# Optimization experiments

Hardware: AMD Instinct MI355X
Metric: run time of the kernel (lower is better)

The kernel has to match this reference:

```python
import jax, jax.numpy as jnp
import numpy as np

H = 50  # LSTM units
T = 10  # NUMBARS
F = 5   # input features
B = 131072


def _lstm(x, W, U, b):
    """Keras-default LSTM. x: [B,T,Fin], W: [Fin,4H], U: [H,4H], b: [4H].
    Gate order i,f,g(c),o; sigmoid recurrent act, tanh cell act, zero init state.
    Returns (all_h [B,T,H], last_h [B,H])."""
    Bn = x.shape[0]
    h0 = jnp.zeros((Bn, H), x.dtype)
    c0 = jnp.zeros((Bn, H), x.dtype)

    def step(carry, xt):
        h, c = carry
        z = xt @ W + h @ U + b  # [B,4H]
        i, f, g, o = jnp.split(z, 4, axis=-1)
        i = jax.nn.sigmoid(i)
        f = jax.nn.sigmoid(f)
        g = jnp.tanh(g)
        o = jax.nn.sigmoid(o)
        c_new = f * c + i * g
        h_new = o * jnp.tanh(c_new)
        return (h_new, c_new), h_new

    (h_last, _), hs = jax.lax.scan(step, (h0, c0), jnp.swapaxes(x, 0, 1))
    return jnp.swapaxes(hs, 0, 1), h_last


def setup_inputs() -> dict:
    key = jax.random.key(0)
    ks = jax.random.split(key, 16)
    d = {"x": jax.random.normal(ks[0], (B, T, F), dtype=jnp.float32)}
    in_dims = [F, H, H, H]
    for l in range(4):
        s_in = 1.0 / np.sqrt(in_dims[l])
        s_h = 1.0 / np.sqrt(H)
        d[f"W{l+1}"] = jax.random.normal(ks[1 + 3 * l], (in_dims[l], 4 * H), dtype=jnp.float32) * s_in
        d[f"U{l+1}"] = jax.random.normal(ks[2 + 3 * l], (H, 4 * H), dtype=jnp.float32) * s_h
        # Keras unit_forget_bias: forget-gate bias = 1
        b = jnp.zeros((4 * H,), jnp.float32).at[H:2 * H].set(1.0)
        d[f"b{l+1}"] = b
    d["Wd1"] = jax.random.normal(ks[13], (H, 50), dtype=jnp.float32) * (1.0 / np.sqrt(H))
    d["bd1"] = jnp.zeros((50,), jnp.float32)
    d["Wd2"] = jax.random.normal(ks[14], (50, 1), dtype=jnp.float32) * (1.0 / np.sqrt(50))
    d["bd2"] = jnp.zeros((1,), jnp.float32)
    return d


def reference(x, W1, U1, b1, W2, U2, b2, W3, U3, b3, W4, U4, b4, Wd1, bd1, Wd2, bd2):
    # Dropout layers are identity at inference (Keras default training=False).
    h, _ = _lstm(x, W1, U1, b1)
    h, _ = _lstm(h, W2, U2, b2)
    h, _ = _lstm(h, W3, U3, b3)
    _, h = _lstm(h, W4, U4, b4)        # return_sequences=False -> last h [B,H]
    h = h @ Wd1 + bd1                   # Dense(50), linear activation
    out = jax.nn.sigmoid(h @ Wd2 + bd2) # Dense(1, sigmoid) -> [B,1]
    return out
```

## Files before the change

### kernel.cpp

```cpp
#include <hip/hip_runtime.h>


typedef __attribute__((ext_vector_type(8))) short short8;
typedef __attribute__((ext_vector_type(4))) float floatx4;
typedef __attribute__((ext_vector_type(2))) float float2v;
typedef unsigned short u16;
typedef unsigned int u32;

constexpr int H_ = 50, T_ = 10, F_ = 5;
constexpr int MTILE = 64;
constexpr int BLKT = 256;
constexpr float LOG2E = 1.4426950408889634f;

__device__ __forceinline__ float rcp_(float x) { return __builtin_amdgcn_rcpf(x); }
__device__ __forceinline__ float exp2_(float x) { return __builtin_amdgcn_exp2f(x); }
__device__ __forceinline__ float sig_nat(float x) {
  return rcp_(1.0f + exp2_(-LOG2E * x));
}

__device__ __forceinline__ u16 f2bf(float f) {
  union { float f; unsigned u; } v; v.f = f;
  unsigned r = v.u + 0x7FFFu + ((v.u >> 16) & 1u);
  return (u16)(r >> 16);
}
__device__ __forceinline__ float bf2f(u16 s) {
  union { unsigned u; float f; } v; v.u = ((unsigned)s) << 16;
  return v.f;
}
__device__ __forceinline__ unsigned pk_bf16(float a, float b) {
  return (unsigned)f2bf(a) | ((unsigned)f2bf(b) << 16);
}

__global__ void prep_kernel(
    const float* W1, const float* U1, const float* b1, const float* W2,
    const float* U2, const float* b2, const float* W3, const float* U3,
    const float* b3, const float* W4, const float* U4, const float* b4,
    const float* Wd1, const float* bd1, const float* Wd2, const float* bd2,
    u16* Wpp, float* biasP, float* vdense) {
  int idx = blockIdx.x * blockDim.x + threadIdx.x;
  const float* Wt[4] = {W1, W2, W3, W4};
  const float* Ut[4] = {U1, U2, U3, U4};
  const float* bt[4] = {b1, b2, b3, b4};
  const int fin[4] = {F_, H_, H_, H_};
  if (idx < 4 * 32768) {
    int l = idx >> 15, r = idx & 32767;
    int j = r & 7, lane = (r >> 3) & 63, w = (r >> 9) & 3, gI = (r >> 11) & 3,
        kt = r >> 13;
    int row = kt * 32 + (lane >> 4) * 8 + j;
    int u = w * 16 + (lane & 15);
    float val = 0.0f;
    if (u < H_) {
      if (row < 64) {
        if (row < fin[l]) val = Wt[l][row * 200 + gI * H_ + u];
      } else {
        int rr = row - 64;
        if (rr < H_) val = Ut[l][rr * 200 + gI * H_ + u];
      }
    }
    val *= (gI == 2) ? (2.0f * LOG2E) : (-LOG2E);
    Wpp[idx] = f2bf(val);
  } else if (idx < 4 * 32768 + 1024) {
    int r = idx - 4 * 32768;
    int l = r >> 8, q = r & 255, gI = q >> 6, u = q & 63;
    float val = (u < H_) ? bt[l][gI * H_ + u] : 0.0f;
    biasP[r] = val * ((gI == 2) ? (2.0f * LOG2E) : (-LOG2E));
  } else if (idx < 4 * 32768 + 1024 + 51) {
    int u = idx - (4 * 32768 + 1024);
    if (u < H_) {
      float s = 0.0f;
      for (int n = 0; n < H_; ++n) s += Wd1[u * H_ + n] * Wd2[n];
      vdense[u] = s;
    } else {
      float s = bd2[0];
      for (int n = 0; n < H_; ++n) s += bd1[n] * Wd2[n];
      vdense[50] = s;
    }
  }
}

template <bool FIRST, bool LAST>
__global__ __launch_bounds__(BLKT, 2) void lstm_mfma(
    const float* __restrict__ x0, u16* hbuf, const u16* __restrict__ Wpp,
    const float* __restrict__ biasP, int nblk, const float* __restrict__ vdense,
    float* __restrict__ out) {
  __shared__ __align__(16) u16 A[8192];
  const int tid = threadIdx.x;
  const int w = tid >> 6, lane = tid & 63;
  const int np = lane & 15, quad = lane >> 4;
  const int blk = blockIdx.x;
  const int b0 = blk * MTILE;
  const int u = w * 16 + np;

  short8 bfr[4][4];
#pragma unroll
  for (int kt = 0; kt < 4; ++kt)
#pragma unroll
    for (int gI = 0; gI < 4; ++gI)
      bfr[kt][gI] = *(const short8*)&Wpp[(((kt * 4 + gI) * 4 + w) * 64 + lane) * 8];

  float bv[4];
#pragma unroll
  for (int gI = 0; gI < 4; ++gI) bv[gI] = biasP[gI * 64 + u];

  for (int i = tid; i < 4096; i += BLKT) ((u32*)A)[i] = 0;

  float2v cst[8];
#pragma unroll
  for (int i = 0; i < 8; ++i) cst[i] = float2v{0.0f, 0.0f};

  short8 rx0, rx1;
  if constexpr (!FIRST) {
    const u16* s0 = hbuf + ((size_t)0 * nblk + blk) * 4096;
    rx0 = *(const short8*)(s0 + (size_t)tid * 8);
    rx1 = *(const short8*)(s0 + (size_t)(tid + 256) * 8);
  }

  const int kt_u = 2 + (w >> 1);
  const int cbase = ((kt_u * 4 + ((w & 1) * 2 + (np >> 3))) * 16 + quad * 4) * 8 + (np & 7);

  __syncthreads();

#pragma unroll 1
  for (int t = 0; t < T_; ++t) {
    if constexpr (!FIRST) {
      {
        int hc = tid, mt = hc >> 7, kk = (hc >> 6) & 1, rest = hc & 63;
        *(short8*)&A[((mt * 4 + kk) * 64 + rest) * 8] = rx0;
      }
      {
        int hc = tid + 256, mt = hc >> 7, kk = (hc >> 6) & 1, rest = hc & 63;
        *(short8*)&A[((mt * 4 + kk) * 64 + rest) * 8] = rx1;
      }
      if (t + 1 < T_) {
        const u16* s1 = hbuf + ((size_t)(t + 1) * nblk + blk) * 4096;
        rx0 = *(const short8*)(s1 + (size_t)tid * 8);
        rx1 = *(const short8*)(s1 + (size_t)(tid + 256) * 8);
      }
    } else {
      for (int e = tid; e < MTILE * F_; e += BLKT) {
        int row = e / F_, k = e - row * F_;
        int mt = row >> 4, rr = row & 15;
        A[(mt * 256 + rr) * 8 + k] =
            f2bf(x0[(size_t)(b0 + row) * (T_ * F_) + t * F_ + k]);
      }
    }
    __syncthreads();

    floatx4 acc[4][4];
#pragma unroll
    for (int mt = 0; mt < 4; ++mt)
#pragma unroll
      for (int gI = 0; gI < 4; ++gI)
        acc[mt][gI] = floatx4{bv[gI], bv[gI], bv[gI], bv[gI]};

#pragma unroll
    for (int kt = 0; kt < 4; ++kt) {
      if (FIRST && kt == 1) continue;
#pragma unroll
      for (int mt = 0; mt < 4; ++mt) {
        short8 af = *(const short8*)&A[(((mt * 4 + kt) * 4 + quad) * 16 + np) * 8];
#pragma unroll
        for (int gI = 0; gI < 4; ++gI)
          acc[mt][gI] = __builtin_amdgcn_mfma_f32_16x16x32_bf16(
              af, bfr[kt][gI], acc[mt][gI], 0, 0, 0);
      }
    }
    __syncthreads();

#pragma unroll
    for (int mt = 0; mt < 4; ++mt) {
#pragma unroll
      for (int p = 0; p < 2; ++p) {
        float2v di = {exp2_(acc[mt][0][2 * p]), exp2_(acc[mt][0][2 * p + 1])};
        float2v df = {exp2_(acc[mt][1][2 * p]), exp2_(acc[mt][1][2 * p + 1])};
        float2v dg = {exp2_(acc[mt][2][2 * p]), exp2_(acc[mt][2][2 * p + 1])};
        float2v do_ = {exp2_(acc[mt][3][2 * p]), exp2_(acc[mt][3][2 * p + 1])};
        di += 1.0f; df += 1.0f; dg += 1.0f; do_ += 1.0f;
        float2v m1 = di * df, m2 = do_ * dg;
        float2v P = m1 * m2;
        float Rs = rcp_(P.x * P.y);
        float2v R = {Rs * P.y, Rs * P.x};
        float2v i_ = (df * m2) * R;
        float2v f_ = (di * m2) * R;
        float2v o_ = (m1 * dg) * R;
        float2v g_ = 1.0f - 2.0f * ((m1 * do_) * R);
        float2v cn = f_ * cst[mt * 2 + p] + i_ * g_;
        cst[mt * 2 + p] = cn;
        float2v s = cn * (2.0f * LOG2E);
        float2v dc = {exp2_(s.x), exp2_(s.y)};
        dc += 1.0f;
        float Rc = rcp_(dc.x * dc.y);
        float2v tc = 1.0f - 2.0f * float2v{Rc * dc.y, Rc * dc.x};
        float2v h = o_ * tc;
        unsigned pk = pk_bf16(h.x, h.y);
        int a0 = cbase + mt * 2048 + (2 * p) * 8;
        A[a0] = (u16)pk;
        A[a0 + 8] = (u16)(pk >> 16);
      }
    }

    if constexpr (!LAST) {
      u16* dst = hbuf + ((size_t)t * nblk + blk) * 4096;
#pragma unroll
      for (int rep = 0; rep < 2; ++rep) {
        int e = lane + 64 * rep;
        int mt = e >> 5, rem = e & 31, qp = rem >> 4, rr = rem & 15;
        int quad_u = (w & 1) * 2 + qp;
        int ldsc = ((mt * 4 + kt_u) * 4 + quad_u) * 16 + rr;
        int hch = ((mt * 2 + (w >> 1)) * 4 + quad_u) * 16 + rr;
        *(short8*)&dst[(size_t)hch * 8] = *(const short8*)&A[ldsc * 8];
      }
    }
  }

  if constexpr (LAST) {
    __syncthreads();
    if (tid < MTILE) {
      int mt = tid >> 4, rr = tid & 15;
      float s = vdense[50];
      for (int k = 0; k < H_; ++k) {
        int ktu = 2 + (k >> 5), qd = (k & 31) >> 3, j = k & 7;
        s += bf2f(A[(((mt * 4 + ktu) * 4 + qd) * 16 + rr) * 8 + j]) * vdense[k];
      }
      out[b0 + tid] = sig_nat(s);
    }
  }
}

extern "C" void kernel_launch(void* const* d_in, const int* in_sizes, int n_in,
                              void* d_out, int out_size, void* d_ws,
                              size_t ws_size, hipStream_t stream) {
  const float* x = (const float*)d_in[0];
  const float* W1 = (const float*)d_in[1];
  const float* U1 = (const float*)d_in[2];
  const float* b1 = (const float*)d_in[3];
  const float* W2 = (const float*)d_in[4];
  const float* U2 = (const float*)d_in[5];
  const float* b2 = (const float*)d_in[6];
  const float* W3 = (const float*)d_in[7];
  const float* U3 = (const float*)d_in[8];
  const float* b3 = (const float*)d_in[9];
  const float* W4 = (const float*)d_in[10];
  const float* U4 = (const float*)d_in[11];
  const float* b4 = (const float*)d_in[12];
  const float* Wd1 = (const float*)d_in[13];
  const float* bd1 = (const float*)d_in[14];
  const float* Wd2 = (const float*)d_in[15];
  const float* bd2 = (const float*)d_in[16];

  const int Bn = in_sizes[0] / (T_ * F_);
  const int nblk = Bn / MTILE;
  char* ws = (char*)d_ws;
  u16* hbuf = (u16*)ws;
  size_t off = (size_t)T_ * nblk * 4096 * sizeof(u16);
  u16* Wpp = (u16*)(ws + off);
  float* biasP = (float*)(ws + off + 262144);
  float* vdense = (float*)(ws + off + 262144 + 4096);
  float* out = (float*)d_out;

  prep_kernel<<<(4 * 32768 + 1024 + 51 + 255) / 256, 256, 0, stream>>>(
      W1, U1, b1, W2, U2, b2, W3, U3, b3, W4, U4, b4, Wd1, bd1, Wd2, bd2, Wpp,
      biasP, vdense);

  dim3 grid(nblk), blkd(BLKT);
  lstm_mfma<true, false><<<grid, blkd, 0, stream>>>(
      x, hbuf, Wpp + 0 * 32768, biasP + 0 * 256, nblk, vdense, nullptr);
  lstm_mfma<false, false><<<grid, blkd, 0, stream>>>(
      nullptr, hbuf, Wpp + 1 * 32768, biasP + 1 * 256, nblk, vdense, nullptr);
  lstm_mfma<false, false><<<grid, blkd, 0, stream>>>(
      nullptr, hbuf, Wpp + 2 * 32768, biasP + 2 * 256, nblk, vdense, nullptr);
  lstm_mfma<false, true><<<grid, blkd, 0, stream>>>(
      nullptr, hbuf, Wpp + 3 * 32768, biasP + 3 * 256, nblk, vdense, out);
}
```

Baseline: 572.2 us.

## Fuse all four LSTM layers into one kernel keeping hidden sequences in LDS

Replaces four per-layer kernel launches that pass hidden sequences through a global bf16 buffer with a single kernel. Each block keeps all ten timesteps of hidden state in shared memory and runs the layers back to back, overwriting each timestep slot in place. The tile shrinks from 64 to 32 rows with a launch bound of three blocks per CU. This removes global round-trips and launch overhead, at the cost of more shared memory per block, fewer rows per MFMA batch, and per-layer weight reloads.

```diff
diff --git a/kernel.cpp b/kernel.cpp
--- a/kernel.cpp
+++ b/kernel.cpp
@@ -8,7 +8,7 @@
 typedef unsigned int u32;
 
 constexpr int H_ = 50, T_ = 10, F_ = 5;
-constexpr int MTILE = 64;
+constexpr int MTILE = 32;
 constexpr int BLKT = 256;
 constexpr float LOG2E = 1.4426950408889634f;
 
@@ -78,152 +78,147 @@
   }
 }
 
-template <bool FIRST, bool LAST>
-__global__ __launch_bounds__(BLKT, 2) void lstm_mfma(
-    const float* __restrict__ x0, u16* hbuf, const u16* __restrict__ Wpp,
-    const float* __restrict__ biasP, int nblk, const float* __restrict__ vdense,
+__global__ __launch_bounds__(BLKT, 3) void lstm_fused(
+    const float* __restrict__ x0, const u16* __restrict__ Wpp,
+    const float* __restrict__ biasP, const float* __restrict__ vdense,
     float* __restrict__ out) {
-  __shared__ __align__(16) u16 A[8192];
+  __shared__ __align__(16) u16 buf[T_ * 2048];
+  __shared__ __align__(16) u16 xb[T_ * 256];
+  __shared__ __align__(16) u16 zc[8];
+
   const int tid = threadIdx.x;
   const int w = tid >> 6, lane = tid & 63;
   const int np = lane & 15, quad = lane >> 4;
-  const int blk = blockIdx.x;
-  const int b0 = blk * MTILE;
+  const int b0 = blockIdx.x * MTILE;
   const int u = w * 16 + np;
 
-  short8 bfr[4][4];
-#pragma unroll
-  for (int kt = 0; kt < 4; ++kt)
-#pragma unroll
-    for (int gI = 0; gI < 4; ++gI)
-      bfr[kt][gI] = *(const short8*)&Wpp[(((kt * 4 + gI) * 4 + w) * 64 + lane) * 8];
-
-  float bv[4];
-#pragma unroll
-  for (int gI = 0; gI < 4; ++gI) bv[gI] = biasP[gI * 64 + u];
-
-  for (int i = tid; i < 4096; i += BLKT) ((u32*)A)[i] = 0;
-
-  float2v cst[8];
-#pragma unroll
-  for (int i = 0; i < 8; ++i) cst[i] = float2v{0.0f, 0.0f};
-
-  short8 rx0, rx1;
-  if constexpr (!FIRST) {
-    const u16* s0 = hbuf + ((size_t)0 * nblk + blk) * 4096;
-    rx0 = *(const short8*)(s0 + (size_t)tid * 8);
-    rx1 = *(const short8*)(s0 + (size_t)(tid + 256) * 8);
-  }
-
-  const int kt_u = 2 + (w >> 1);
-  const int cbase = ((kt_u * 4 + ((w & 1) * 2 + (np >> 3))) * 16 + quad * 4) * 8 + (np & 7);
-
+  for (int i = tid; i < T_ * 128; i += BLKT) ((u32*)xb)[i] = 0;
+  if (tid < 4) ((u32*)zc)[tid] = 0;
   __syncthreads();
 
+  for (int e = tid; e < MTILE * 50; e += BLKT) {
+    int row = e / 50, q = e - row * 50;
+    int t = q / 5, f = q - t * 5;
+    xb[t * 256 + row * 8 + f] = f2bf(x0[(size_t)(b0 + row) * 50 + q]);
+  }
+  __syncthreads();
+
+  const int rbase = quad * 128 + np * 8;
+  const int cb0 = (w >> 1) * 512 + ((w & 1) * 2 + (np >> 3)) * 128 + quad * 32 + (np & 7);
+
+  float2v cst[4];
+
 #pragma unroll 1
-  for (int t = 0; t < T_; ++t) {
-    if constexpr (!FIRST) {
-      {
-        int hc = tid, mt = hc >> 7, kk = (hc >> 6) & 1, rest = hc & 63;
-        *(short8*)&A[((mt * 4 + kk) * 64 + rest) * 8] = rx0;
-      }
-      {
-        int hc = tid + 256, mt = hc >> 7, kk = (hc >> 6) & 1, rest = hc & 63;
-        *(short8*)&A[((mt * 4 + kk) * 64 + rest) * 8] = rx1;
-      }
-      if (t + 1 < T_) {
-        const u16* s1 = hbuf + ((size_t)(t + 1) * nblk + blk) * 4096;
-        rx0 = *(const short8*)(s1 + (size_t)tid * 8);
-        rx1 = *(const short8*)(s1 + (size_t)(tid + 256) * 8);
-      }
-    } else {
-      for (int e = tid; e < MTILE * F_; e += BLKT) {
-        int row = e / F_, k = e - row * F_;
-        int mt = row >> 4, rr = row & 15;
-        A[(mt * 256 + rr) * 8 + k] =
-            f2bf(x0[(size_t)(b0 + row) * (T_ * F_) + t * F_ + k]);
-      }
-    }
-    __syncthreads();
-
-    floatx4 acc[4][4];
-#pragma unroll
-    for (int mt = 0; mt < 4; ++mt)
-#pragma unroll
-      for (int gI = 0; gI < 4; ++gI)
-        acc[mt][gI] = floatx4{bv[gI], bv[gI], bv[gI], bv[gI]};
-
-#pragma unroll
-    for (int kt = 0; kt < 4; ++kt) {
-      if (FIRST && kt == 1) continue;
-#pragma unroll
-      for (int mt = 0; mt < 4; ++mt) {
-        short8 af = *(const short8*)&A[(((mt * 4 + kt) * 4 + quad) * 16 + np) * 8];
-#pragma unroll
-        for (int gI = 0; gI < 4; ++gI)
-          acc[mt][gI] = __builtin_amdgcn_mfma_f32_16x16x32_bf16(
-              af, bfr[kt][gI], acc[mt][gI], 0, 0, 0);
-      }
-    }
-    __syncthreads();
-
-#pragma unroll
-    for (int mt = 0; mt < 4; ++mt) {
-#pragma unroll
-      for (int p = 0; p < 2; ++p) {
-        float2v di = {exp2_(acc[mt][0][2 * p]), exp2_(acc[mt][0][2 * p + 1])};
-        float2v df = {exp2_(acc[mt][1][2 * p]), exp2_(acc[mt][1][2 * p + 1])};
-        float2v dg = {exp2_(acc[mt][2][2 * p]), exp2_(acc[mt][2][2 * p + 1])};
-        float2v do_ = {exp2_(acc[mt][3][2 * p]), exp2_(acc[mt][3][2 * p + 1])};
-        di += 1.0f; df += 1.0f; dg += 1.0f; do_ += 1.0f;
-        float2v m1 = di * df, m2 = do_ * dg;
-        float2v P = m1 * m2;
-        float Rs = rcp_(P.x * P.y);
-        float2v R = {Rs * P.y, Rs * P.x};
-        float2v i_ = (df * m2) * R;
-        float2v f_ = (di * m2) * R;
-        float2v o_ = (m1 * dg) * R;
-        float2v g_ = 1.0f - 2.0f * ((m1 * do_) * R);
-        float2v cn = f_ * cst[mt * 2 + p] + i_ * g_;
-        cst[mt * 2 + p] = cn;
-        float2v s = cn * (2.0f * LOG2E);
-        float2v dc = {exp2_(s.x), exp2_(s.y)};
-        dc += 1.0f;
-        float Rc = rcp_(dc.x * dc.y);
-        float2v tc = 1.0f - 2.0f * float2v{Rc * dc.y, Rc * dc.x};
-        float2v h = o_ * tc;
-        unsigned pk = pk_bf16(h.x, h.y);
-        int a0 = cbase + mt * 2048 + (2 * p) * 8;
-        A[a0] = (u16)pk;
-        A[a0 + 8] = (u16)(pk >> 16);
-      }
-    }
-
-    if constexpr (!LAST) {
-      u16* dst = hbuf + ((size_t)t * nblk + blk) * 4096;
-#pragma unroll
-      for (int rep = 0; rep < 2; ++rep) {
-        int e = lane + 64 * rep;
-        int mt = e >> 5, rem = e & 31, qp = rem >> 4, rr = rem & 15;
-        int quad_u = (w & 1) * 2 + qp;
-        int ldsc = ((mt * 4 + kt_u) * 4 + quad_u) * 16 + rr;
-        int hch = ((mt * 2 + (w >> 1)) * 4 + quad_u) * 16 + rr;
-        *(short8*)&dst[(size_t)hch * 8] = *(const short8*)&A[ldsc * 8];
-      }
-    }
-  }
-
-  if constexpr (LAST) {
-    __syncthreads();
-    if (tid < MTILE) {
-      int mt = tid >> 4, rr = tid & 15;
-      float s = vdense[50];
-      for (int k = 0; k < H_; ++k) {
-        int ktu = 2 + (k >> 5), qd = (k & 31) >> 3, j = k & 7;
-        s += bf2f(A[(((mt * 4 + ktu) * 4 + qd) * 16 + rr) * 8 + j]) * vdense[k];
-      }
-      out[b0 + tid] = sig_nat(s);
-    }
+  for (int l = 0; l < 4; ++l) {
+    const u16* wp = Wpp + l * 32768;
+    short8 bfr[4][4];
+#pragma unroll
+    for (int kt = 0; kt < 4; ++kt)
+#pragma unroll
+      for (int g = 0; g < 4; ++g)
+        bfr[kt][g] = *(const short8*)&wp[(((kt * 4 + g) * 4 + w) * 64 + lane) * 8];
+    float bv[4];
+#pragma unroll
+    for (int g = 0; g < 4; ++g) bv[g] = biasP[l * 256 + g * 64 + u];
+#pragma unroll
+    for (int i = 0; i < 4; ++i) cst[i] = float2v{0.0f, 0.0f};
+
+#pragma unroll 1
+    for (int t = 0; t < T_; ++t) {
+      u16* bt = &buf[t * 2048];
+      const u16* bp = &buf[(t == 0 ? 0 : (t - 1)) * 2048];
+
+      floatx4 acc[2][4];
+#pragma unroll
+      for (int mt = 0; mt < 2; ++mt)
+#pragma unroll
+        for (int g = 0; g < 4; ++g)
+          acc[mt][g] = floatx4{bv[g], bv[g], bv[g], bv[g]};
+
+      if (l == 0) {
+#pragma unroll
+        for (int mt = 0; mt < 2; ++mt) {
+          const u16* ap = (quad == 0) ? &xb[t * 256 + (mt * 16 + np) * 8] : zc;
+          short8 af = *(const short8*)ap;
+#pragma unroll
+          for (int g = 0; g < 4; ++g)
+            acc[mt][g] = __builtin_amdgcn_mfma_f32_16x16x32_bf16(
+                af, bfr[0][g], acc[mt][g], 0, 0, 0);
+        }
+      } else {
+#pragma unroll
+        for (int mt = 0; mt < 2; ++mt) {
+          short8 a0 = *(const short8*)&bt[mt * 1024 + rbase];
+          short8 a1 = *(const short8*)&bt[mt * 1024 + 512 + rbase];
+#pragma unroll
+          for (int g = 0; g < 4; ++g) {
+            acc[mt][g] = __builtin_amdgcn_mfma_f32_16x16x32_bf16(
+                a0, bfr[0][g], acc[mt][g], 0, 0, 0);
+            acc[mt][g] = __builtin_amdgcn_mfma_f32_16x16x32_bf16(
+                a1, bfr[1][g], acc[mt][g], 0, 0, 0);
+          }
+        }
+      }
+      if (t > 0) {
+#pragma unroll
+        for (int mt = 0; mt < 2; ++mt) {
+          short8 h0 = *(const short8*)&bp[mt * 1024 + rbase];
+          short8 h1 = *(const short8*)&bp[mt * 1024 + 512 + rbase];
+#pragma unroll
+          for (int g = 0; g < 4; ++g) {
+            acc[mt][g] = __builtin_amdgcn_mfma_f32_16x16x32_bf16(
+                h0, bfr[2][g], acc[mt][g], 0, 0, 0);
+            acc[mt][g] = __builtin_amdgcn_mfma_f32_16x16x32_bf16(
+                h1, bfr[3][g], acc[mt][g], 0, 0, 0);
+          }
+        }
+      }
+      if (l > 0) __syncthreads();
+
+#pragma unroll
+      for (int mt = 0; mt < 2; ++mt) {
+#pragma unroll
+        for (int p = 0; p < 2; ++p) {
+          float2v di = {exp2_(acc[mt][0][2 * p]), exp2_(acc[mt][0][2 * p + 1])};
+          float2v df = {exp2_(acc[mt][1][2 * p]), exp2_(acc[mt][1][2 * p + 1])};
+          float2v dg = {exp2_(acc[mt][2][2 * p]), exp2_(acc[mt][2][2 * p + 1])};
+          float2v do_ = {exp2_(acc[mt][3][2 * p]), exp2_(acc[mt][3][2 * p + 1])};
+          di += 1.0f; df += 1.0f; dg += 1.0f; do_ += 1.0f;
+          float2v m1 = di * df, m2 = do_ * dg;
+          float2v P = m1 * m2;
+          float Rs = rcp_(P.x * P.y);
+          float2v R = {Rs * P.y, Rs * P.x};
+          float2v i_ = (df * m2) * R;
+          float2v f_ = (di * m2) * R;
+          float2v o_ = (m1 * dg) * R;
+          float2v g_ = 1.0f - 2.0f * ((m1 * do_) * R);
+          float2v cn = f_ * cst[mt * 2 + p] + i_ * g_;
+          cst[mt * 2 + p] = cn;
+          float2v s = cn * (2.0f * LOG2E);
+          float2v dc = {exp2_(s.x), exp2_(s.y)};
+          dc += 1.0f;
+          float Rc = rcp_(dc.x * dc.y);
+          float2v tc = 1.0f - 2.0f * float2v{Rc * dc.y, Rc * dc.x};
+          float2v h = o_ * tc;
+          unsigned pk = pk_bf16(h.x, h.y);
+          int a0 = cb0 + mt * 1024 + p * 16;
+          bt[a0] = (u16)pk;
+          bt[a0 + 8] = (u16)(pk >> 16);
+        }
+      }
+      __syncthreads();
+    }
+  }
+
+  if (tid < MTILE) {
+    int mt = tid >> 4, rr = tid & 15;
+    const u16* b9 = &buf[9 * 2048];
+    float s = vdense[50];
+    for (int k = 0; k < H_; ++k) {
+      int kk = k >> 5, qd = (k & 31) >> 3, j = k & 7;
+      s += bf2f(b9[mt * 1024 + kk * 512 + qd * 128 + rr * 8 + j]) * vdense[k];
+    }
+    out[b0 + tid] = sig_nat(s);
   }
 }
 
@@ -251,24 +246,14 @@
   const int Bn = in_sizes[0] / (T_ * F_);
   const int nblk = Bn / MTILE;
   char* ws = (char*)d_ws;
-  u16* hbuf = (u16*)ws;
-  size_t off = (size_t)T_ * nblk * 4096 * sizeof(u16);
-  u16* Wpp = (u16*)(ws + off);
-  float* biasP = (float*)(ws + off + 262144);
-  float* vdense = (float*)(ws + off + 262144 + 4096);
+  u16* Wpp = (u16*)ws;
+  float* biasP = (float*)(ws + 262144);
+  float* vdense = (float*)(ws + 262144 + 4096);
   float* out = (float*)d_out;
 
   prep_kernel<<<(4 * 32768 + 1024 + 51 + 255) / 256, 256, 0, stream>>>(
       W1, U1, b1, W2, U2, b2, W3, U3, b3, W4, U4, b4, Wd1, bd1, Wd2, bd2, Wpp,
       biasP, vdense);
 
-  dim3 grid(nblk), blkd(BLKT);
-  lstm_mfma<true, false><<<grid, blkd, 0, stream>>>(
-      x, hbuf, Wpp + 0 * 32768, biasP + 0 * 256, nblk, vdense, nullptr);
-  lstm_mfma<false, false><<<grid, blkd, 0, stream>>>(
-      nullptr, hbuf, Wpp + 1 * 32768, biasP + 1 * 256, nblk, vdense, nullptr);
-  lstm_mfma<false, false><<<grid, blkd, 0, stream>>>(
-      nullptr, hbuf, Wpp + 2 * 32768, biasP + 2 * 256, nblk, vdense, nullptr);
-  lstm_mfma<false, true><<<grid, blkd, 0, stream>>>(
-      nullptr, hbuf, Wpp + 3 * 32768, biasP + 3 * 256, nblk, vdense, out);
-}
+  lstm_fused<<<dim3(nblk), dim3(BLKT), 0, stream>>>(x, Wpp, biasP, vdense, out);
+}
```

After: 487.9 us. 1.17x faster.
